# Performance work log

Measured on AMD Instinct MI355X. Metric: run time of the kernel, lower is better.

Reference implementation:

```python
import jax, jax.numpy as jnp
import numpy as np

NEG_SLOPE = 0.2  # PyG GATConv default negative_slope


def _gat_layer(x, src, dst, W, att_src, att_dst, bias, heads, out_c, concat, num_nodes):
    # x: [N, F_in]; W: [F_in, heads*out_c]
    h = (x @ W).reshape(num_nodes, heads, out_c)          # [N, H, C]
    a_src = (h * att_src[None]).sum(-1)                    # [N, H]
    a_dst = (h * att_dst[None]).sum(-1)                    # [N, H]
    e = jax.nn.leaky_relu(a_src[src] + a_dst[dst], NEG_SLOPE)  # [E, H]
    # segment softmax over incoming edges of each destination node
    e_max = jax.ops.segment_max(e, dst, num_segments=num_nodes)  # [N, H]
    e_exp = jnp.exp(e - e_max[dst])                        # [E, H]
    denom = jax.ops.segment_sum(e_exp, dst, num_segments=num_nodes)  # [N, H]
    alpha = e_exp / (denom[dst] + 1e-16)                   # [E, H]
    out = jax.ops.segment_sum(alpha[:, :, None] * h[src], dst, num_segments=num_nodes)  # [N, H, C]
    if concat:
        out = out.reshape(num_nodes, heads * out_c)
    else:
        out = out.mean(axis=1)
    return out + bias


def setup_inputs() -> dict:
    key = jax.random.key(0)
    ks = jax.random.split(key, 8)
    N, E = 50000, 800000
    x = jax.random.normal(ks[0], (N, 3), dtype=jnp.float32)
    edge_index = jax.random.randint(ks[1], (2, E), 0, N, dtype=jnp.int64)
    # layer 1: 3 -> 64 per head, 4 heads, concat
    W1 = jax.random.normal(ks[2], (3, 256), dtype=jnp.float32) * 0.3
    att_src1 = jax.random.normal(ks[3], (4, 64), dtype=jnp.float32) * 0.1
    att_dst1 = jax.random.normal(ks[4], (4, 64), dtype=jnp.float32) * 0.1
    b1 = jnp.zeros((256,), dtype=jnp.float32)
    # layer 2: 256 -> 128, 1 head, mean (concat=False)
    W2 = jax.random.normal(ks[5], (256, 128), dtype=jnp.float32) * 0.06
    att_src2 = jax.random.normal(ks[6], (1, 128), dtype=jnp.float32) * 0.1
    att_dst2 = jax.random.normal(ks[7], (1, 128), dtype=jnp.float32) * 0.1
    b2 = jnp.zeros((128,), dtype=jnp.float32)
    return {"x": x, "edge_index": edge_index, "W1": W1, "att_src1": att_src1,
            "att_dst1": att_dst1, "b1": b1, "W2": W2, "att_src2": att_src2,
            "att_dst2": att_dst2, "b2": b2}


def reference(x, edge_index, W1, att_src1, att_dst1, b1, W2, att_src2, att_dst2, b2):
    N = x.shape[0]
    loops = jnp.arange(N, dtype=edge_index.dtype)
    src = jnp.concatenate([edge_index[0], loops])  # PyG add_self_loops=True
    dst = jnp.concatenate([edge_index[1], loops])
    h = _gat_layer(x, src, dst, W1, att_src1, att_dst1, b1, heads=4, out_c=64,
                   concat=True, num_nodes=N)          # [N, 256]
    h = jax.nn.elu(h)
    out = _gat_layer(h, src, dst, W2, att_src2, att_dst2, b2, heads=1, out_c=128,
                     concat=False, num_nodes=N)       # [N, 128]
    return out
```

## Files before the change

### kernel.cpp

```cpp
#include <hip/hip_runtime.h>

#define NEG_SLOPE 0.2f
typedef unsigned short ushort_t;
typedef __attribute__((ext_vector_type(8))) short bf16x8;
typedef __attribute__((ext_vector_type(4))) float f32x4;

__device__ __forceinline__ float lrelu(float z){ return z > 0.f ? z : NEG_SLOPE * z; }

__device__ __forceinline__ ushort_t bf16_rn(float x){
  union { float f; unsigned u; } v; v.f = x;
  unsigned r = v.u + 0x7FFF + ((v.u >> 16) & 1);
  return (ushort_t)(r >> 16);
}
__device__ __forceinline__ float bf16_to_f(ushort_t h){
  union { unsigned u; float f; } v; v.u = ((unsigned)h) << 16;
  return v.f;
}

__device__ __forceinline__ float4 ld_h2q(const ushort_t* __restrict__ h2, int s, int r){
  uint2 u = *(const uint2*)&h2[(size_t)s * 128 + r * 4];
  float4 f;
  f.x = bf16_to_f((ushort_t)(u.x & 0xffffu));
  f.y = bf16_to_f((ushort_t)(u.x >> 16));
  f.z = bf16_to_f((ushort_t)(u.y & 0xffffu));
  f.w = bf16_to_f((ushort_t)(u.y >> 16));
  return f;
}

__global__ __launch_bounds__(256) void k_prep(
    const float* __restrict__ W1, const float* __restrict__ att_src1, const float* __restrict__ att_dst1,
    const float* __restrict__ W2, const float* __restrict__ x,
    ushort_t* __restrict__ w2hi, ushort_t* __restrict__ w2lo,
    float* __restrict__ uv, float4* __restrict__ xp, int N)
{
  if (blockIdx.x >= 17) {
    int n = (blockIdx.x - 17) * 256 + threadIdx.x;
    if (n < N) {
      float4 v = {x[n * 3], x[n * 3 + 1], x[n * 3 + 2], 0.f};
      xp[n] = v;
    }
    return;
  }
  int gid = blockIdx.x * 256 + threadIdx.x;
  if (gid < 4096) {
    int kc = gid >> 9, g = (gid >> 7) & 3, n = gid & 127;
    #pragma unroll
    for (int e = 0; e < 8; ++e) {
      int k = kc * 32 + g * 8 + e;
      float w = W2[k * 128 + n];
      ushort_t hi = bf16_rn(w);
      ushort_t lo = bf16_rn(w - bf16_to_f(hi));
      w2hi[(size_t)gid * 8 + e] = hi;
      w2lo[(size_t)gid * 8 + e] = lo;
    }
  } else if (gid < 4120) {
    int j = gid - 4096;
    int jj = j % 12;
    int k = jj >> 2, h = jj & 3;
    const float* att = (j < 12) ? att_src1 : att_dst1;
    float s = 0.f;
    for (int c = 0; c < 64; ++c) s += W1[k * 256 + h * 64 + c] * att[h * 64 + c];
    uv[j] = s;
  }
}

__global__ __launch_bounds__(256) void k_hist(
    const int* __restrict__ ei, int E, int NB, int* __restrict__ hist)
{
  __shared__ int h[512];
  int t = threadIdx.x;
  for (int i = t; i < NB; i += 256) h[i] = 0;
  __syncthreads();
  int e0 = (blockIdx.x * 256 + t) * 8;
  #pragma unroll
  for (int k = 0; k < 8; ++k) {
    int e = e0 + k;
    if (e < E) atomicAdd(&h[ei[E + e] >> 7], 1);
  }
  __syncthreads();
  for (int i = t; i < NB; i += 256)
    if (h[i]) atomicAdd(&hist[i], h[i]);
}

__global__ __launch_bounds__(512) void k_scanB(
    const int* __restrict__ hist, int NB, int E,
    int* __restrict__ cbase, int* __restrict__ cursorB)
{
  __shared__ int s[512];
  int t = threadIdx.x;
  int v = (t < NB) ? hist[t] : 0;
  s[t] = v;
  __syncthreads();
  for (int off = 1; off < 512; off <<= 1) {
    int u = (t >= off) ? s[t - off] : 0;
    __syncthreads();
    s[t] += u;
    __syncthreads();
  }
  if (t < NB) {
    int excl = s[t] - v;
    cbase[t] = excl;
    cursorB[t] = excl;
  }
  if (t == NB - 1) cbase[NB] = s[t];
}

__global__ __launch_bounds__(256) void k_scatter(
    const int* __restrict__ ei, int E, int NB,
    int* __restrict__ cursorB, uint2* __restrict__ pairs)
{
  __shared__ int lcnt[512];
  __shared__ int gb[512];
  int t = threadIdx.x;
  for (int i = t; i < NB; i += 256) lcnt[i] = 0;
  __syncthreads();
  int e0 = (blockIdx.x * 256 + t) * 8;
  int lrank[8], dst[8], src[8];
  #pragma unroll
  for (int k = 0; k < 8; ++k) {
    int e = e0 + k;
    if (e < E) {
      src[k] = ei[e];
      dst[k] = ei[E + e];
      lrank[k] = atomicAdd(&lcnt[dst[k] >> 7], 1);
    }
  }
  __syncthreads();
  for (int i = t; i < NB; i += 256)
    gb[i] = lcnt[i] ? atomicAdd(&cursorB[i], lcnt[i]) : 0;
  __syncthreads();
  #pragma unroll
  for (int k = 0; k < 8; ++k) {
    int e = e0 + k;
    if (e < E) {
      uint2 pr; pr.x = (unsigned)src[k]; pr.y = (unsigned)dst[k];
      pairs[gb[dst[k] >> 7] + lrank[k]] = pr;
    }
  }
}

__global__ __launch_bounds__(256) void k_bucket(
    const uint2* __restrict__ pairs, const int* __restrict__ cbase,
    int N, int NB, int E,
    int* __restrict__ offsets, int* __restrict__ srclist)
{
  __shared__ int lc[128];
  __shared__ int lexcl[128];
  __shared__ int lcur[128];
  __shared__ int s[256];
  int b = blockIdx.x;
  int t = threadIdx.x;
  int n0 = b << 7;
  int nloc = min(128, N - n0);
  int ebeg = cbase[b], eend = cbase[b + 1];
  int Gb = ebeg + n0;

  if (t < 128) lc[t] = 0;
  __syncthreads();
  for (int e = ebeg + t; e < eend; e += 256)
    atomicAdd(&lc[pairs[e].y & 127], 1);
  __syncthreads();

  int v = (t < nloc) ? lc[t] + 1 : 0;
  s[t] = v;
  __syncthreads();
  for (int off = 1; off < 256; off <<= 1) {
    int u = (t >= off) ? s[t - off] : 0;
    __syncthreads();
    s[t] += u;
    __syncthreads();
  }
  if (t < nloc) {
    int excl = s[t] - v;
    lexcl[t] = excl;
    lcur[t] = excl;
    offsets[n0 + t] = Gb + excl;
  }
  __syncthreads();

  for (int e = ebeg + t; e < eend; e += 256) {
    uint2 pr = pairs[e];
    int i = pr.y & 127;
    int pos = atomicAdd(&lcur[i], 1);
    srclist[Gb + pos] = (int)pr.x;
  }
  if (t < nloc) srclist[Gb + lexcl[t] + lc[t]] = n0 + t;
  if (b == NB - 1 && t == 0) offsets[N] = E + N;
}

__global__ __launch_bounds__(256) void k_agg1(
    const float4* __restrict__ xp, const float* __restrict__ uv,
    const int* __restrict__ offsets, const int* __restrict__ srclist,
    float* __restrict__ X, int N)
{
  int t = threadIdx.x;
  int lane = t & 63;
  int g = lane >> 5, r = lane & 31;
  int n = blockIdx.x * 8 + (t >> 6) * 2 + g;
  if (n >= N) return;

  float us[12], ud[12];
  #pragma unroll
  for (int j = 0; j < 12; ++j) { us[j] = uv[j]; ud[j] = uv[12 + j]; }

  float4 xn = xp[n];
  float ad0 = xn.x * ud[0] + xn.y * ud[4] + xn.z * ud[8];
  float ad1 = xn.x * ud[1] + xn.y * ud[5] + xn.z * ud[9];
  float ad2 = xn.x * ud[2] + xn.y * ud[6] + xn.z * ud[10];
  float ad3 = xn.x * ud[3] + xn.y * ud[7] + xn.z * ud[11];

  int off = offsets[n];
  int deg = offsets[n + 1] - off;
  int c0 = min(deg, 32);
  float a0 = -1e30f, a1 = -1e30f, a2 = -1e30f, a3 = -1e30f;
  float x0 = 0.f, x1 = 0.f, x2 = 0.f;
  if (r < c0) {
    int s = srclist[off + r];
    float4 xs = xp[s];
    x0 = xs.x; x1 = xs.y; x2 = xs.z;
    a0 = lrelu(x0 * us[0] + x1 * us[4] + x2 * us[8]  + ad0);
    a1 = lrelu(x0 * us[1] + x1 * us[5] + x2 * us[9]  + ad1);
    a2 = lrelu(x0 * us[2] + x1 * us[6] + x2 * us[10] + ad2);
    a3 = lrelu(x0 * us[3] + x1 * us[7] + x2 * us[11] + ad3);
  }
  float m0 = a0, m1 = a1, m2 = a2, m3 = a3;
  for (int base = 32; base < deg; base += 32) {
    if (r < deg - base) {
      int s = srclist[off + base + r];
      float4 xs = xp[s];
      m0 = fmaxf(m0, lrelu(xs.x * us[0] + xs.y * us[4] + xs.z * us[8]  + ad0));
      m1 = fmaxf(m1, lrelu(xs.x * us[1] + xs.y * us[5] + xs.z * us[9]  + ad1));
      m2 = fmaxf(m2, lrelu(xs.x * us[2] + xs.y * us[6] + xs.z * us[10] + ad2));
      m3 = fmaxf(m3, lrelu(xs.x * us[3] + xs.y * us[7] + xs.z * us[11] + ad3));
    }
  }
  #pragma unroll
  for (int msk = 16; msk > 0; msk >>= 1) {
    m0 = fmaxf(m0, __shfl_xor(m0, msk, 32)); m1 = fmaxf(m1, __shfl_xor(m1, msk, 32));
    m2 = fmaxf(m2, __shfl_xor(m2, msk, 32)); m3 = fmaxf(m3, __shfl_xor(m3, msk, 32));
  }

  float e0 = (r < c0) ? __expf(a0 - m0) : 0.f;
  float e1 = (r < c0) ? __expf(a1 - m1) : 0.f;
  float e2 = (r < c0) ? __expf(a2 - m2) : 0.f;
  float e3 = (r < c0) ? __expf(a3 - m3) : 0.f;
  float d0 = e0, d1 = e1, d2 = e2, d3 = e3;
  float xa00 = e0 * x0, xa01 = e1 * x0, xa02 = e2 * x0, xa03 = e3 * x0;
  float xa10 = e0 * x1, xa11 = e1 * x1, xa12 = e2 * x1, xa13 = e3 * x1;
  float xa20 = e0 * x2, xa21 = e1 * x2, xa22 = e2 * x2, xa23 = e3 * x2;

  for (int base = 32; base < deg; base += 32) {
    if (r < deg - base) {
      int s = srclist[off + base + r];
      float4 xs = xp[s];
      float ee0 = __expf(lrelu(xs.x * us[0] + xs.y * us[4] + xs.z * us[8]  + ad0) - m0);
      float ee1 = __expf(lrelu(xs.x * us[1] + xs.y * us[5] + xs.z * us[9]  + ad1) - m1);
      float ee2 = __expf(lrelu(xs.x * us[2] + xs.y * us[6] + xs.z * us[10] + ad2) - m2);
      float ee3 = __expf(lrelu(xs.x * us[3] + xs.y * us[7] + xs.z * us[11] + ad3) - m3);
      d0 += ee0; d1 += ee1; d2 += ee2; d3 += ee3;
      xa00 += ee0 * xs.x; xa01 += ee1 * xs.x; xa02 += ee2 * xs.x; xa03 += ee3 * xs.x;
      xa10 += ee0 * xs.y; xa11 += ee1 * xs.y; xa12 += ee2 * xs.y; xa13 += ee3 * xs.y;
      xa20 += ee0 * xs.z; xa21 += ee1 * xs.z; xa22 += ee2 * xs.z; xa23 += ee3 * xs.z;
    }
  }

  #pragma unroll
  for (int msk = 16; msk > 0; msk >>= 1) {
    d0 += __shfl_xor(d0, msk, 32); d1 += __shfl_xor(d1, msk, 32);
    d2 += __shfl_xor(d2, msk, 32); d3 += __shfl_xor(d3, msk, 32);
    xa00 += __shfl_xor(xa00, msk, 32); xa01 += __shfl_xor(xa01, msk, 32);
    xa02 += __shfl_xor(xa02, msk, 32); xa03 += __shfl_xor(xa03, msk, 32);
    xa10 += __shfl_xor(xa10, msk, 32); xa11 += __shfl_xor(xa11, msk, 32);
    xa12 += __shfl_xor(xa12, msk, 32); xa13 += __shfl_xor(xa13, msk, 32);
    xa20 += __shfl_xor(xa20, msk, 32); xa21 += __shfl_xor(xa21, msk, 32);
    xa22 += __shfl_xor(xa22, msk, 32); xa23 += __shfl_xor(xa23, msk, 32);
  }

  if (r < 16) {
    int j = r;
    float v =
      j == 0 ? d0 : j == 1 ? d1 : j == 2 ? d2 : j == 3 ? d3 :
      j == 4 ? xa00 : j == 5 ? xa01 : j == 6 ? xa02 : j == 7 ? xa03 :
      j == 8 ? xa10 : j == 9 ? xa11 : j == 10 ? xa12 : j == 11 ? xa13 :
      j == 12 ? xa20 : j == 13 ? xa21 : j == 14 ? xa22 : xa23;
    X[(size_t)n * 16 + j] = v;
  }
}

__global__ __launch_bounds__(256) void k_mm2(
    const float* __restrict__ Xc, const float* __restrict__ W1, const float* __restrict__ b1,
    const ushort_t* __restrict__ w2hi, const ushort_t* __restrict__ w2lo,
    const float* __restrict__ att_src2, const float* __restrict__ att_dst2,
    ushort_t* __restrict__ h2, float* __restrict__ a_src2, float* __restrict__ a_dst2, int N)
{
  __shared__ ushort_t h1hi[32 * 256];
  __shared__ ushort_t h1lo[32 * 256];
  __shared__ float Xs[512];
  __shared__ float W1s[768];
  __shared__ float b1s[256];
  __shared__ float invs[128];
  __shared__ float sred_s[32][4];
  __shared__ float sred_d[32][4];

  int t = threadIdx.x;
  int n0 = blockIdx.x * 32;

  for (int i = t; i < 768; i += 256) W1s[i] = W1[i];
  b1s[t] = b1[t];
  for (int i = t; i < 512; i += 256) {
    int idx = n0 * 16 + i;
    Xs[i] = (idx < N * 16) ? Xc[idx] : 0.f;
  }
  __syncthreads();
  if (t < 128) invs[t] = 1.f / (Xs[(t >> 2) * 16 + (t & 3)] + 1e-16f);
  __syncthreads();

  {
    int c = t, h = t >> 6;
    float w0 = W1s[c], w1 = W1s[256 + c], w2v = W1s[512 + c], bb = b1s[c];
    #pragma unroll 4
    for (int i = 0; i < 32; ++i) {
      float inv = invs[i * 4 + h];
      float X0 = Xs[i * 16 + 4 + h] * inv;
      float X1 = Xs[i * 16 + 8 + h] * inv;
      float X2 = Xs[i * 16 + 12 + h] * inv;
      float v = fmaf(w0, X0, fmaf(w1, X1, fmaf(w2v, X2, bb)));
      v = v > 0.f ? v : __expf(v) - 1.f;
      ushort_t hi = bf16_rn(v);
      ushort_t lo = bf16_rn(v - bf16_to_f(hi));
      int idx = (i * 256 + c) ^ ((i & 7) << 3);
      h1hi[idx] = hi;
      h1lo[idx] = lo;
    }
  }
  __syncthreads();

  int lane = t & 63;
  int w = t >> 6;
  int lm = lane & 15, lg = lane >> 4;

  f32x4 acc[2][2];
  f32x4 zz = {0.f, 0.f, 0.f, 0.f};
  acc[0][0] = zz; acc[0][1] = zz; acc[1][0] = zz; acc[1][1] = zz;

  int rowA0 = lm, rowA1 = 16 + lm;
  int swz0 = (rowA0 & 7) << 3, swz1 = (rowA1 & 7) << 3;

  for (int kc = 0; kc < 8; ++kc) {
    int ks = kc * 32 + lg * 8;
    int ia0 = (rowA0 * 256 + ks) ^ swz0;
    int ia1 = (rowA1 * 256 + ks) ^ swz1;
    bf16x8 ah0 = *(const bf16x8*)&h1hi[ia0];
    bf16x8 al0 = *(const bf16x8*)&h1lo[ia0];
    bf16x8 ah1 = *(const bf16x8*)&h1hi[ia1];
    bf16x8 al1 = *(const bf16x8*)&h1lo[ia1];
    size_t bb0 = ((size_t)((kc * 4 + lg) * 128) + (w * 32 + lm)) * 8;
    size_t bb1 = bb0 + 16 * 8;
    bf16x8 bh0 = *(const bf16x8*)&w2hi[bb0];
    bf16x8 bl0 = *(const bf16x8*)&w2lo[bb0];
    bf16x8 bh1 = *(const bf16x8*)&w2hi[bb1];
    bf16x8 bl1 = *(const bf16x8*)&w2lo[bb1];

    acc[0][0] = __builtin_amdgcn_mfma_f32_16x16x32_bf16(ah0, bh0, acc[0][0], 0, 0, 0);
    acc[0][1] = __builtin_amdgcn_mfma_f32_16x16x32_bf16(ah0, bh1, acc[0][1], 0, 0, 0);
    acc[1][0] = __builtin_amdgcn_mfma_f32_16x16x32_bf16(ah1, bh0, acc[1][0], 0, 0, 0);
    acc[1][1] = __builtin_amdgcn_mfma_f32_16x16x32_bf16(ah1, bh1, acc[1][1], 0, 0, 0);
    acc[0][0] = __builtin_amdgcn_mfma_f32_16x16x32_bf16(ah0, bl0, acc[0][0], 0, 0, 0);
    acc[0][1] = __builtin_amdgcn_mfma_f32_16x16x32_bf16(ah0, bl1, acc[0][1], 0, 0, 0);
    acc[1][0] = __builtin_amdgcn_mfma_f32_16x16x32_bf16(ah1, bl0, acc[1][0], 0, 0, 0);
    acc[1][1] = __builtin_amdgcn_mfma_f32_16x16x32_bf16(ah1, bl1, acc[1][1], 0, 0, 0);
    acc[0][0] = __builtin_amdgcn_mfma_f32_16x16x32_bf16(al0, bh0, acc[0][0], 0, 0, 0);
    acc[0][1] = __builtin_amdgcn_mfma_f32_16x16x32_bf16(al0, bh1, acc[0][1], 0, 0, 0);
    acc[1][0] = __builtin_amdgcn_mfma_f32_16x16x32_bf16(al1, bh0, acc[1][0], 0, 0, 0);
    acc[1][1] = __builtin_amdgcn_mfma_f32_16x16x32_bf16(al1, bh1, acc[1][1], 0, 0, 0);
  }

  float as0 = att_src2[w * 32 + lm], as1 = att_src2[w * 32 + 16 + lm];
  float ad0 = att_dst2[w * 32 + lm], ad1 = att_dst2[w * 32 + 16 + lm];
  #pragma unroll
  for (int mi = 0; mi < 2; ++mi) {
    float ps[4], pd[4];
    #pragma unroll
    for (int rg = 0; rg < 4; ++rg) {
      float c0v = acc[mi][0][rg], c1v = acc[mi][1][rg];
      int nrow = n0 + mi * 16 + lg * 4 + rg;
      if (nrow < N) {
        h2[(size_t)nrow * 128 + w * 32 + lm] = bf16_rn(c0v);
        h2[(size_t)nrow * 128 + w * 32 + 16 + lm] = bf16_rn(c1v);
      }
      ps[rg] = c0v * as0 + c1v * as1;
      pd[rg] = c0v * ad0 + c1v * ad1;
    }
    #pragma unroll
    for (int rg = 0; rg < 4; ++rg) {
      #pragma unroll
      for (int m = 8; m >= 1; m >>= 1) {
        ps[rg] += __shfl_xor(ps[rg], m, 64);
        pd[rg] += __shfl_xor(pd[rg], m, 64);
      }
      if (lm == 0) {
        int row = mi * 16 + lg * 4 + rg;
        sred_s[row][w] = ps[rg];
        sred_d[row][w] = pd[rg];
      }
    }
  }
  __syncthreads();
  if (t < 32) {
    int n = n0 + t;
    if (n < N) {
      a_src2[n] = sred_s[t][0] + sred_s[t][1] + sred_s[t][2] + sred_s[t][3];
      a_dst2[n] = sred_d[t][0] + sred_d[t][1] + sred_d[t][2] + sred_d[t][3];
    }
  }
}

__global__ __launch_bounds__(256) void k_agg2(
    const ushort_t* __restrict__ h2, const float* __restrict__ b2,
    const float* __restrict__ a_src2, const float* __restrict__ a_dst2,
    const int* __restrict__ offsets, const int* __restrict__ srclist,
    float* __restrict__ out, int N)
{
  int t = threadIdx.x, lane = t & 63;
  int g = lane >> 5, r = lane & 31;
  int n = blockIdx.x * 8 + (t >> 6) * 2 + g;
  if (n >= N) return;
  int off = offsets[n], deg = offsets[n + 1] - off;
  float adn = a_dst2[n];

  int c0 = min(deg, 32);
  int s_l = 0; float a_l = -1e30f;
  if (r < c0) { s_l = srclist[off + r]; a_l = lrelu(a_src2[s_l] + adn); }
  float m = a_l;
  for (int base = 32; base < deg; base += 32)
    if (r < deg - base) m = fmaxf(m, lrelu(a_src2[srclist[off + base + r]] + adn));
  #pragma unroll
  for (int msk = 16; msk > 0; msk >>= 1) m = fmaxf(m, __shfl_xor(m, msk, 32));

  float e_l = (r < c0) ? __expf(a_l - m) : 0.f;
  float den_p = e_l;
  float4 acc = {0.f, 0.f, 0.f, 0.f};

  int j = 0;
  for (; j + 4 <= c0; j += 4) {
    int   sA = __shfl(s_l, j, 32),     sB = __shfl(s_l, j + 1, 32);
    int   sC = __shfl(s_l, j + 2, 32), sD = __shfl(s_l, j + 3, 32);
    float eA = __shfl(e_l, j, 32),     eB = __shfl(e_l, j + 1, 32);
    float eC = __shfl(e_l, j + 2, 32), eD = __shfl(e_l, j + 3, 32);
    float4 hA = ld_h2q(h2, sA, r);
    float4 hB = ld_h2q(h2, sB, r);
    float4 hC = ld_h2q(h2, sC, r);
    float4 hD = ld_h2q(h2, sD, r);
    acc.x += eA * hA.x + eB * hB.x + eC * hC.x + eD * hD.x;
    acc.y += eA * hA.y + eB * hB.y + eC * hC.y + eD * hD.y;
    acc.z += eA * hA.z + eB * hB.z + eC * hC.z + eD * hD.z;
    acc.w += eA * hA.w + eB * hB.w + eC * hC.w + eD * hD.w;
  }
  for (; j < c0; ++j) {
    int sA = __shfl(s_l, j, 32);
    float eA = __shfl(e_l, j, 32);
    float4 hA = ld_h2q(h2, sA, r);
    acc.x += eA * hA.x; acc.y += eA * hA.y; acc.z += eA * hA.z; acc.w += eA * hA.w;
  }
  for (int base = 32; base < deg; base += 32) {
    int rem = min(32, deg - base);
    int sl2 = 0; float el2 = 0.f;
    if (r < rem) { sl2 = srclist[off + base + r]; el2 = __expf(lrelu(a_src2[sl2] + adn) - m); }
    den_p += el2;
    for (int q = 0; q < rem; ++q) {
      int s = __shfl(sl2, q, 32);
      float e = __shfl(el2, q, 32);
      float4 hv = ld_h2q(h2, s, r);
      acc.x += e * hv.x; acc.y += e * hv.y; acc.z += e * hv.z; acc.w += e * hv.w;
    }
  }
  #pragma unroll
  for (int msk = 16; msk > 0; msk >>= 1) den_p += __shfl_xor(den_p, msk, 32);
  float inv = 1.f / (den_p + 1e-16f);
  float4 bb = *(const float4*)&b2[r * 4];
  float4 o = {acc.x * inv + bb.x, acc.y * inv + bb.y, acc.z * inv + bb.z, acc.w * inv + bb.w};
  *(float4*)&out[(size_t)n * 128 + r * 4] = o;
}

extern "C" void kernel_launch(void* const* d_in, const int* in_sizes, int n_in,
                              void* d_out, int out_size, void* d_ws, size_t ws_size,
                              hipStream_t stream)
{
  const float* x        = (const float*)d_in[0];
  const int*   ei       = (const int*)d_in[1];
  const float* W1       = (const float*)d_in[2];
  const float* att_src1 = (const float*)d_in[3];
  const float* att_dst1 = (const float*)d_in[4];
  const float* b1       = (const float*)d_in[5];
  const float* W2       = (const float*)d_in[6];
  const float* att_src2 = (const float*)d_in[7];
  const float* att_dst2 = (const float*)d_in[8];
  const float* b2       = (const float*)d_in[9];
  float* out = (float*)d_out;

  int N = in_sizes[0] / 3;
  int E = in_sizes[1] / 2;
  int NB = (N + 127) >> 7;

  char* p = (char*)d_ws;
  auto alloc = [&](size_t bytes) -> char* {
    char* r = p;
    p += (bytes + 255) & ~(size_t)255;
    return r;
  };
  float*    uv      = (float*)alloc(24 * 4);
  ushort_t* w2hi    = (ushort_t*)alloc(32768 * 2);
  ushort_t* w2lo    = (ushort_t*)alloc(32768 * 2);
  float4*   xp      = (float4*)alloc((size_t)N * 16);
  float*    a_src2  = (float*)alloc((size_t)N * 4);
  float*    a_dst2  = (float*)alloc((size_t)N * 4);
  int*      hist    = (int*)alloc(512 * 4);
  int*      cbase   = (int*)alloc(513 * 4);
  int*      cursorB = (int*)alloc(512 * 4);
  uint2*    pairs   = (uint2*)alloc((size_t)E * 8);
  int*      offsets = (int*)alloc((size_t)(N + 1) * 4);
  int*      srclist = (int*)alloc((size_t)(E + N) * 4);
  float*    Xc      = (float*)alloc((size_t)16 * N * 4);
  ushort_t* h2      = (ushort_t*)alloc((size_t)128 * N * 2);

  int nEB = (E + 2047) / 2048;

  hipMemsetAsync(hist, 0, 512 * 4, stream);
  k_prep<<<17 + (N + 255) / 256, 256, 0, stream>>>(W1, att_src1, att_dst1, W2, x, w2hi, w2lo, uv, xp, N);
  k_hist<<<nEB, 256, 0, stream>>>(ei, E, NB, hist);
  k_scanB<<<1, 512, 0, stream>>>(hist, NB, E, cbase, cursorB);
  k_scatter<<<nEB, 256, 0, stream>>>(ei, E, NB, cursorB, pairs);
  k_bucket<<<NB, 256, 0, stream>>>(pairs, cbase, N, NB, E, offsets, srclist);
  k_agg1<<<(N + 7) / 8, 256, 0, stream>>>(xp, uv, offsets, srclist, Xc, N);
  k_mm2<<<(N + 31) / 32, 256, 0, stream>>>(Xc, W1, b1, w2hi, w2lo, att_src2, att_dst2, h2, a_src2, a_dst2, N);
  k_agg2<<<(N + 7) / 8, 256, 0, stream>>>(h2, b2, a_src2, a_dst2, offsets, srclist, out, N);
}
```

Measured before the change: 208.9 us.

## Fuse histogram into prep kernel, pack edge pairs, vectorize scatter loads

Merges the destination-bucket histogram kernel into the prep kernel as extra blocks, which removes one launch. Source and local destination index are packed into a single 32-bit word (src<<7 | dst&127), halving pairs traffic between scatter and bucket. Edge loads in scatter use int4 vector loads. The packing assumes src fits in 25 bits, and the fused kernel mixes heterogeneous block roles.

Result: no change. 205.0 us (-1.8%).

```diff
diff --git a/kernel.cpp b/kernel.cpp
--- a/kernel.cpp
+++ b/kernel.cpp
@@ -30,48 +30,48 @@
 __global__ __launch_bounds__(256) void k_prep(
     const float* __restrict__ W1, const float* __restrict__ att_src1, const float* __restrict__ att_dst1,
     const float* __restrict__ W2, const float* __restrict__ x,
+    const int* __restrict__ ei, int E, int NB, int NPX,
     ushort_t* __restrict__ w2hi, ushort_t* __restrict__ w2lo,
-    float* __restrict__ uv, float4* __restrict__ xp, int N)
-{
-  if (blockIdx.x >= 17) {
-    int n = (blockIdx.x - 17) * 256 + threadIdx.x;
+    float* __restrict__ uv, float4* __restrict__ xp, int* __restrict__ hist, int N)
+{
+  __shared__ int h[512];
+  int b = blockIdx.x;
+  int t = threadIdx.x;
+  if (b < 17) {
+    int gid = b * 256 + t;
+    if (gid < 4096) {
+      int kc = gid >> 9, g = (gid >> 7) & 3, n = gid & 127;
+      #pragma unroll
+      for (int e = 0; e < 8; ++e) {
+        int k = kc * 32 + g * 8 + e;
+        float w = W2[k * 128 + n];
+        ushort_t hi = bf16_rn(w);
+        ushort_t lo = bf16_rn(w - bf16_to_f(hi));
+        w2hi[(size_t)gid * 8 + e] = hi;
+        w2lo[(size_t)gid * 8 + e] = lo;
+      }
+    } else if (gid < 4120) {
+      int j = gid - 4096;
+      int jj = j % 12;
+      int k = jj >> 2, hh = jj & 3;
+      const float* att = (j < 12) ? att_src1 : att_dst1;
+      float s = 0.f;
+      for (int c = 0; c < 64; ++c) s += W1[k * 256 + hh * 64 + c] * att[hh * 64 + c];
+      uv[j] = s;
+    }
+    return;
+  }
+  if (b < 17 + NPX) {
+    int n = (b - 17) * 256 + t;
     if (n < N) {
       float4 v = {x[n * 3], x[n * 3 + 1], x[n * 3 + 2], 0.f};
       xp[n] = v;
     }
     return;
   }
-  int gid = blockIdx.x * 256 + threadIdx.x;
-  if (gid < 4096) {
-    int kc = gid >> 9, g = (gid >> 7) & 3, n = gid & 127;
-    #pragma unroll
-    for (int e = 0; e < 8; ++e) {
-      int k = kc * 32 + g * 8 + e;
-      float w = W2[k * 128 + n];
-      ushort_t hi = bf16_rn(w);
-      ushort_t lo = bf16_rn(w - bf16_to_f(hi));
-      w2hi[(size_t)gid * 8 + e] = hi;
-      w2lo[(size_t)gid * 8 + e] = lo;
-    }
-  } else if (gid < 4120) {
-    int j = gid - 4096;
-    int jj = j % 12;
-    int k = jj >> 2, h = jj & 3;
-    const float* att = (j < 12) ? att_src1 : att_dst1;
-    float s = 0.f;
-    for (int c = 0; c < 64; ++c) s += W1[k * 256 + h * 64 + c] * att[h * 64 + c];
-    uv[j] = s;
-  }
-}
-
-__global__ __launch_bounds__(256) void k_hist(
-    const int* __restrict__ ei, int E, int NB, int* __restrict__ hist)
-{
-  __shared__ int h[512];
-  int t = threadIdx.x;
   for (int i = t; i < NB; i += 256) h[i] = 0;
   __syncthreads();
-  int e0 = (blockIdx.x * 256 + t) * 8;
+  int e0 = ((b - 17 - NPX) * 256 + t) * 8;
   #pragma unroll
   for (int k = 0; k < 8; ++k) {
     int e = e0 + k;
@@ -107,40 +107,50 @@
 
 __global__ __launch_bounds__(256) void k_scatter(
     const int* __restrict__ ei, int E, int NB,
-    int* __restrict__ cursorB, uint2* __restrict__ pairs)
+    int* __restrict__ cursorB, unsigned* __restrict__ pairs)
 {
   __shared__ int lcnt[512];
   __shared__ int gb[512];
   int t = threadIdx.x;
   for (int i = t; i < NB; i += 256) lcnt[i] = 0;
   __syncthreads();
+
   int e0 = (blockIdx.x * 256 + t) * 8;
   int lrank[8], dst[8], src[8];
-  #pragma unroll
-  for (int k = 0; k < 8; ++k) {
-    int e = e0 + k;
-    if (e < E) {
-      src[k] = ei[e];
-      dst[k] = ei[E + e];
-      lrank[k] = atomicAdd(&lcnt[dst[k] >> 7], 1);
-    }
-  }
+  if (e0 + 8 <= E) {
+    int4 s0 = *(const int4*)&ei[e0];
+    int4 s1 = *(const int4*)&ei[e0 + 4];
+    int4 d0 = *(const int4*)&ei[E + e0];
+    int4 d1 = *(const int4*)&ei[E + e0 + 4];
+    src[0]=s0.x; src[1]=s0.y; src[2]=s0.z; src[3]=s0.w;
+    src[4]=s1.x; src[5]=s1.y; src[6]=s1.z; src[7]=s1.w;
+    dst[0]=d0.x; dst[1]=d0.y; dst[2]=d0.z; dst[3]=d0.w;
+    dst[4]=d1.x; dst[5]=d1.y; dst[6]=d1.z; dst[7]=d1.w;
+  } else {
+    #pragma unroll
+    for (int k = 0; k < 8; ++k) {
+      int e = e0 + k;
+      src[k] = (e < E) ? ei[e] : 0;
+      dst[k] = (e < E) ? ei[E + e] : 0;
+    }
+  }
+  #pragma unroll
+  for (int k = 0; k < 8; ++k)
+    if (e0 + k < E) lrank[k] = atomicAdd(&lcnt[dst[k] >> 7], 1);
+
   __syncthreads();
   for (int i = t; i < NB; i += 256)
     gb[i] = lcnt[i] ? atomicAdd(&cursorB[i], lcnt[i]) : 0;
   __syncthreads();
-  #pragma unroll
-  for (int k = 0; k < 8; ++k) {
-    int e = e0 + k;
-    if (e < E) {
-      uint2 pr; pr.x = (unsigned)src[k]; pr.y = (unsigned)dst[k];
-      pairs[gb[dst[k] >> 7] + lrank[k]] = pr;
-    }
-  }
+
+  #pragma unroll
+  for (int k = 0; k < 8; ++k)
+    if (e0 + k < E)
+      pairs[gb[dst[k] >> 7] + lrank[k]] = ((unsigned)src[k] << 7) | (unsigned)(dst[k] & 127);
 }
 
 __global__ __launch_bounds__(256) void k_bucket(
-    const uint2* __restrict__ pairs, const int* __restrict__ cbase,
+    const unsigned* __restrict__ pairs, const int* __restrict__ cbase,
     int N, int NB, int E,
     int* __restrict__ offsets, int* __restrict__ srclist)
 {
@@ -158,7 +168,7 @@
   if (t < 128) lc[t] = 0;
   __syncthreads();
   for (int e = ebeg + t; e < eend; e += 256)
-    atomicAdd(&lc[pairs[e].y & 127], 1);
+    atomicAdd(&lc[pairs[e] & 127], 1);
   __syncthreads();
 
   int v = (t < nloc) ? lc[t] + 1 : 0;
@@ -179,10 +189,10 @@
   __syncthreads();
 
   for (int e = ebeg + t; e < eend; e += 256) {
-    uint2 pr = pairs[e];
-    int i = pr.y & 127;
+    unsigned pr = pairs[e];
+    int i = (int)(pr & 127u);
     int pos = atomicAdd(&lcur[i], 1);
-    srclist[Gb + pos] = (int)pr.x;
+    srclist[Gb + pos] = (int)(pr >> 7);
   }
   if (t < nloc) srclist[Gb + lexcl[t] + lc[t]] = n0 + t;
   if (b == NB - 1 && t == 0) offsets[N] = E + N;
@@ -501,6 +511,8 @@
   int N = in_sizes[0] / 3;
   int E = in_sizes[1] / 2;
   int NB = (N + 127) >> 7;
+  int NPX = (N + 255) / 256;
+  int nEB = (E + 2047) / 2048;
 
   char* p = (char*)d_ws;
   auto alloc = [&](size_t bytes) -> char* {
@@ -517,17 +529,15 @@
   int*      hist    = (int*)alloc(512 * 4);
   int*      cbase   = (int*)alloc(513 * 4);
   int*      cursorB = (int*)alloc(512 * 4);
-  uint2*    pairs   = (uint2*)alloc((size_t)E * 8);
+  unsigned* pairs   = (unsigned*)alloc((size_t)E * 4);
   int*      offsets = (int*)alloc((size_t)(N + 1) * 4);
   int*      srclist = (int*)alloc((size_t)(E + N) * 4);
   float*    Xc      = (float*)alloc((size_t)16 * N * 4);
   ushort_t* h2      = (ushort_t*)alloc((size_t)128 * N * 2);
 
-  int nEB = (E + 2047) / 2048;
-
   hipMemsetAsync(hist, 0, 512 * 4, stream);
-  k_prep<<<17 + (N + 255) / 256, 256, 0, stream>>>(W1, att_src1, att_dst1, W2, x, w2hi, w2lo, uv, xp, N);
-  k_hist<<<nEB, 256, 0, stream>>>(ei, E, NB, hist);
+  k_prep<<<17 + NPX + nEB, 256, 0, stream>>>(W1, att_src1, att_dst1, W2, x, ei, E, NB, NPX,
+                                             w2hi, w2lo, uv, xp, hist, N);
   k_scanB<<<1, 512, 0, stream>>>(hist, NB, E, cbase, cursorB);
   k_scatter<<<nEB, 256, 0, stream>>>(ei, E, NB, cursorB, pairs);
   k_bucket<<<NB, 256, 0, stream>>>(pairs, cbase, N, NB, E, offsets, srclist);
```
